# Performance work log

Measured on AMD Instinct MI355X. Metric: run time of the kernel, lower is better.

Reference implementation:

```python
import jax, jax.numpy as jnp
import numpy as np

T, H, NH, NKV, HD = 2048, 2048, 16, 4, 128
I, E, TOPK = 4096, 8, 2
EPS = 1e-5
THETA = 10000.0
NEG = -1e9


def rmsnorm(x, w):
    return x * jax.lax.rsqrt(jnp.mean(x * x, axis=-1, keepdims=True) + EPS) * w


def apply_rope(x, pos):
    # neox-style rotary: split head_dim in halves
    half = HD // 2
    inv_freq = 1.0 / (THETA ** (jnp.arange(half, dtype=jnp.float32) / half))
    f = pos.astype(jnp.float32)[:, None] * inv_freq[None, :]      # [T, half]
    cos = jnp.cos(f)[:, None, :]
    sin = jnp.sin(f)[:, None, :]
    x1, x2 = jnp.split(x, 2, axis=-1)
    return jnp.concatenate([x1 * cos - x2 * sin, x2 * cos + x1 * sin], axis=-1)


def setup_inputs() -> dict:
    key = jax.random.key(0)
    ks = jax.random.split(key, 10)
    s = 0.02
    return {
        "positions": jnp.arange(T, dtype=jnp.int32),
        "hidden_states": jax.random.normal(ks[0], (T, H), jnp.float32),
        "residual": jax.random.normal(ks[1], (T, H), jnp.float32),
        "ln1_w": jnp.ones((H,), jnp.float32),
        "ln2_w": jnp.ones((H,), jnp.float32),
        "wq": jax.random.normal(ks[2], (NH * HD, H), jnp.float32) * s,
        "wk": jax.random.normal(ks[3], (NKV * HD, H), jnp.float32) * s,
        "wv": jax.random.normal(ks[4], (NKV * HD, H), jnp.float32) * s,
        "wo": jax.random.normal(ks[5], (H, NH * HD), jnp.float32) * s,
        "gate_w": jax.random.normal(ks[6], (E, H), jnp.float32) * s,
        "w1": jax.random.normal(ks[7], (E, I, H), jnp.float32) * s,
        "w3": jax.random.normal(ks[8], (E, I, H), jnp.float32) * s,
        "w2": jax.random.normal(ks[9], (E, H, I), jnp.float32) * s,
    }


def reference(positions, hidden_states, residual, ln1_w, ln2_w,
              wq, wk, wv, wo, gate_w, w1, w3, w2):
    # fused add + input RMSNorm (vLLM RMSNorm with residual)
    x = hidden_states + residual
    residual = x
    h = rmsnorm(x, ln1_w)

    # attention: QKV proj, RoPE, GQA causal attention, o_proj
    q = (h @ wq.T).reshape(T, NH, HD)
    k = (h @ wk.T).reshape(T, NKV, HD)
    v = (h @ wv.T).reshape(T, NKV, HD)
    q = apply_rope(q, positions)
    k = apply_rope(k, positions)
    rep = NH // NKV
    k = jnp.repeat(k, rep, axis=1)  # [T, NH, HD]
    v = jnp.repeat(v, rep, axis=1)
    scores = jnp.einsum('qhd,khd->hqk', q, k) * (HD ** -0.5)
    causal = jnp.tril(jnp.ones((T, T), bool))
    scores = jnp.where(causal[None, :, :], scores, NEG)
    attn = jax.nn.softmax(scores, axis=-1)
    o = jnp.einsum('hqk,khd->qhd', attn, v).reshape(T, NH * HD)
    o = o @ wo.T

    # fused add + post-attention RMSNorm
    x = o + residual
    residual = x
    h = rmsnorm(x, ln2_w)

    # MoE: router top-k (renormalized) + SwiGLU experts
    logits = h @ gate_w.T                       # [T, E]
    probs = jax.nn.softmax(logits, axis=-1)
    top_w, top_i = jax.lax.top_k(probs, TOPK)
    top_w = top_w / jnp.sum(top_w, axis=-1, keepdims=True)
    coef = jnp.zeros((T, E), h.dtype).at[jnp.arange(T)[:, None], top_i].set(top_w)
    out = jnp.zeros_like(h)
    for e in range(E):
        g = h @ w1[e].T                          # [T, I]
        u = h @ w3[e].T
        out = out + coef[:, e:e + 1] * ((jax.nn.silu(g) * u) @ w2[e].T)
    return (out, residual)
```

## Files before the change

### kernel.cpp

```cpp
#include <hip/hip_runtime.h>
#include <hip/hip_bf16.h>
#include <math.h>


#define T_  2048
#define H_  2048
#define NH  16
#define NKV 4
#define HD  128
#define II_ 4096
#define NE  8
#define EPS 1e-5f
#define PROWS 6144

typedef __bf16 bf16x8 __attribute__((ext_vector_type(8)));
typedef float  f32x4  __attribute__((ext_vector_type(4)));
typedef unsigned short u16;

__device__ __forceinline__ u16 f2b(float f){ __bf16 b = (__bf16)f; return __builtin_bit_cast(u16, b); }
__device__ __forceinline__ float b2f(u16 u){ return (float)__builtin_bit_cast(__bf16, u); }

__device__ __forceinline__ void gll16(const void* g, void* l){
  __builtin_amdgcn_global_load_lds(
      (const __attribute__((address_space(1))) unsigned int*)g,
      (__attribute__((address_space(3))) unsigned int*)l, 16, 0, 0);
}

__global__ __launch_bounds__(256) void mx_cvt_split(const float* __restrict__ s,
                                                    u16* __restrict__ hi,
                                                    u16* __restrict__ lo, int n8)
{
  int i = blockIdx.x*256 + threadIdx.x;
  int stride = gridDim.x*256;
  for (; i < n8; i += stride){
    const f32x4* p = (const f32x4*)s + 2*(size_t)i;
    f32x4 a = p[0], b = p[1];
    uint4 uh, ul;
    u16 h0,h1,h2,h3;
    h0=f2b(a[0]); h1=f2b(a[1]); h2=f2b(a[2]); h3=f2b(a[3]);
    uh.x = (unsigned)h0 | ((unsigned)h1<<16);
    uh.y = (unsigned)h2 | ((unsigned)h3<<16);
    ul.x = (unsigned)f2b(a[0]-b2f(h0)) | ((unsigned)f2b(a[1]-b2f(h1))<<16);
    ul.y = (unsigned)f2b(a[2]-b2f(h2)) | ((unsigned)f2b(a[3]-b2f(h3))<<16);
    h0=f2b(b[0]); h1=f2b(b[1]); h2=f2b(b[2]); h3=f2b(b[3]);
    uh.z = (unsigned)h0 | ((unsigned)h1<<16);
    uh.w = (unsigned)h2 | ((unsigned)h3<<16);
    ul.z = (unsigned)f2b(b[0]-b2f(h0)) | ((unsigned)f2b(b[1]-b2f(h1))<<16);
    ul.w = (unsigned)f2b(b[2]-b2f(h2)) | ((unsigned)f2b(b[3]-b2f(h3))<<16);
    ((uint4*)hi)[i] = uh;
    ((uint4*)lo)[i] = ul;
  }
}

__global__ void mx_rope_table(const int* __restrict__ pos, float* __restrict__ cosT,
                              float* __restrict__ sinT)
{
  int i = blockIdx.x*256 + threadIdx.x;
  int t = i >> 6, d = i & 63;
  float inv = (float)exp(-((double)d/64.0) * 9.210340371976184);
  float f = (float)pos[t] * inv;
  cosT[i] = cosf(f); sinT[i] = sinf(f);
}

__global__ __launch_bounds__(256) void mx_addnorm(
    const float* __restrict__ a, const float* __restrict__ b,
    const float* __restrict__ gam, float* __restrict__ res_out,
    u16* __restrict__ hi, u16* __restrict__ lo,
    float* __restrict__ hf, u16* __restrict__ hbf, int* __restrict__ mz)
{
  int t = blockIdx.x, tid = threadIdx.x;
  if (mz && t == 0 && tid < 8) mz[tid] = 0;
  const float4* A4 = (const float4*)a + (size_t)t*512;
  const float4* B4 = (const float4*)b + (size_t)t*512;
  float4 va = A4[tid], vb = B4[tid];
  float4 x0; x0.x=va.x+vb.x; x0.y=va.y+vb.y; x0.z=va.z+vb.z; x0.w=va.w+vb.w;
  va = A4[tid+256]; vb = B4[tid+256];
  float4 x1; x1.x=va.x+vb.x; x1.y=va.y+vb.y; x1.z=va.z+vb.z; x1.w=va.w+vb.w;
  float ss = x0.x*x0.x + x0.y*x0.y + x0.z*x0.z + x0.w*x0.w
           + x1.x*x1.x + x1.y*x1.y + x1.z*x1.z + x1.w*x1.w;
  #pragma unroll
  for (int d=32; d; d>>=1) ss += __shfl_down(ss, d);
  __shared__ float red[4];
  if ((tid&63)==0) red[tid>>6] = ss;
  __syncthreads();
  ss = red[0]+red[1]+red[2]+red[3];
  float scale = rsqrtf(ss * (1.f/2048.f) + EPS);
  float4* R4 = (float4*)res_out + (size_t)t*512;
  R4[tid] = x0; R4[tid+256] = x1;
  const float4* G4p = (const float4*)gam;
  float4 g0 = G4p[tid], g1 = G4p[tid+256];
  float4 y0; y0.x=x0.x*scale*g0.x; y0.y=x0.y*scale*g0.y; y0.z=x0.z*scale*g0.z; y0.w=x0.w*scale*g0.w;
  float4 y1; y1.x=x1.x*scale*g1.x; y1.y=x1.y*scale*g1.y; y1.z=x1.z*scale*g1.z; y1.w=x1.w*scale*g1.w;
  if (hf){ float4* H4 = (float4*)hf + (size_t)t*512; H4[tid]=y0; H4[tid+256]=y1; }
  if (hi){
    ushort4 uh, ul;
    uh.x=f2b(y0.x); ul.x=f2b(y0.x-b2f(uh.x));
    uh.y=f2b(y0.y); ul.y=f2b(y0.y-b2f(uh.y));
    uh.z=f2b(y0.z); ul.z=f2b(y0.z-b2f(uh.z));
    uh.w=f2b(y0.w); ul.w=f2b(y0.w-b2f(uh.w));
    ((ushort4*)hi)[(size_t)t*512 + tid] = uh; ((ushort4*)lo)[(size_t)t*512 + tid] = ul;
    uh.x=f2b(y1.x); ul.x=f2b(y1.x-b2f(uh.x));
    uh.y=f2b(y1.y); ul.y=f2b(y1.y-b2f(uh.y));
    uh.z=f2b(y1.z); ul.z=f2b(y1.z-b2f(uh.z));
    uh.w=f2b(y1.w); ul.w=f2b(y1.w-b2f(uh.w));
    ((ushort4*)hi)[(size_t)t*512 + tid+256] = uh; ((ushort4*)lo)[(size_t)t*512 + tid+256] = ul;
  }
  if (hbf){
    ushort4 u0; u0.x=f2b(y0.x); u0.y=f2b(y0.y); u0.z=f2b(y0.z); u0.w=f2b(y0.w);
    ushort4 u1; u1.x=f2b(y1.x); u1.y=f2b(y1.y); u1.z=f2b(y1.z); u1.w=f2b(y1.w);
    ((ushort4*)hbf)[(size_t)t*512 + tid] = u0; ((ushort4*)hbf)[(size_t)t*512 + tid+256] = u1;
  }
}

template<int NX, int NY>
__global__ __launch_bounds__(256,2) void mx_gemm3g(
    const u16* __restrict__ Ah, const u16* __restrict__ Al,
    const u16* __restrict__ Bh, const u16* __restrict__ Bl,
    float* __restrict__ C, int ldc, int K)
{
  __shared__ u16 AhS[128*64], AlS[128*64], BhS[128*64], BlS[128*64];
  int bid = blockIdx.x;
  int xcd = bid & 7, j = bid >> 3;
  int x = j % NX, p = j / NX;
  int y = xcd + 8*p;
  int m0 = x*128, n0 = y*128;
  int tid = threadIdx.x;
  int w = tid>>6, lane = tid&63, wr = w>>1, wc = w&1, g = lane>>4, lr = lane&15;
  f32x4 acc[4][4];
  #pragma unroll
  for (int fm=0;fm<4;fm++)
    #pragma unroll
    for (int fn=0;fn<4;fn++) acc[fm][fn] = (f32x4){0.f,0.f,0.f,0.f};

  for (int k0 = 0; k0 < K; k0 += 64) {
    #pragma unroll
    for (int i=0;i<4;i++){
      int c = i*256 + tid, r = c>>3, ch = c&7;
      int sw = ((ch ^ (r&7))<<3);
      int db = (i*256 + w*64)<<3;
      gll16(Ah + (size_t)(m0+r)*K + k0 + sw, &AhS[db]);
      gll16(Al + (size_t)(m0+r)*K + k0 + sw, &AlS[db]);
      gll16(Bh + (size_t)(n0+r)*K + k0 + sw, &BhS[db]);
      gll16(Bl + (size_t)(n0+r)*K + k0 + sw, &BlS[db]);
    }
    __syncthreads();
    #pragma unroll
    for (int kk=0;kk<2;kk++){
      bf16x8 ah[4], al[4], bh[4], bl[4];
      #pragma unroll
      for (int fm=0;fm<4;fm++){
        int r = wr*64 + fm*16 + lr;
        int ch = ((kk<<2)+g) ^ (r&7);
        ah[fm] = *(const bf16x8*)(&AhS[(r<<6)+(ch<<3)]);
        al[fm] = *(const bf16x8*)(&AlS[(r<<6)+(ch<<3)]);
      }
      #pragma unroll
      for (int fn=0;fn<4;fn++){
        int r = wc*64 + fn*16 + lr;
        int ch = ((kk<<2)+g) ^ (r&7);
        bh[fn] = *(const bf16x8*)(&BhS[(r<<6)+(ch<<3)]);
        bl[fn] = *(const bf16x8*)(&BlS[(r<<6)+(ch<<3)]);
      }
      __builtin_amdgcn_s_setprio(1);
      #pragma unroll
      for (int fm=0;fm<4;fm++)
        #pragma unroll
        for (int fn=0;fn<4;fn++){
          acc[fm][fn] = __builtin_amdgcn_mfma_f32_16x16x32_bf16(ah[fm], bh[fn], acc[fm][fn],0,0,0);
          acc[fm][fn] = __builtin_amdgcn_mfma_f32_16x16x32_bf16(ah[fm], bl[fn], acc[fm][fn],0,0,0);
          acc[fm][fn] = __builtin_amdgcn_mfma_f32_16x16x32_bf16(al[fm], bh[fn], acc[fm][fn],0,0,0);
        }
      __builtin_amdgcn_s_setprio(0);
    }
    __syncthreads();
  }
  #pragma unroll
  for (int fm=0;fm<4;fm++)
    #pragma unroll
    for (int fn=0;fn<4;fn++)
      #pragma unroll
      for (int i=0;i<4;i++){
        size_t rg = (size_t)(m0 + wr*64 + fm*16 + g*4 + i);
        int cg = n0 + wc*64 + fn*16 + lr;
        C[rg*ldc + cg] = acc[fm][fn][i];
      }
}

template<int NY>
__global__ __launch_bounds__(256,2) void mx_moe_w13(
    const u16* __restrict__ A,
    const u16* __restrict__ B1, const u16* __restrict__ B3,
    u16* __restrict__ Y,
    const int* __restrict__ row_map, const int* __restrict__ meta)
{
  __shared__ u16 As[128*64], B1s[128*64], B3s[128*64];
  int bid = blockIdx.x;
  int xcd = bid & 7, j = bid >> 3;
  int x = j & 15, p = j >> 4;
  int panel = xcd + 8*p;
  int e = panel / NY, y = panel % NY;
  if (x >= meta[16+e]) return;
  int rowbase = meta[8+e] + (x<<7);
  const u16* B1p = B1 + ((size_t)e*II_ + y*128)*H_;
  const u16* B3p = B3 + ((size_t)e*II_ + y*128)*H_;
  int tid = threadIdx.x;
  int w = tid>>6, lane = tid&63, wr = w>>1, wc = w&1, g = lane>>4, lr = lane&15;

  f32x4 acc1[4][4], acc3[4][4];
  #pragma unroll
  for (int fm=0;fm<4;fm++)
    #pragma unroll
    for (int fn=0;fn<4;fn++){ acc1[fm][fn]=(f32x4){0,0,0,0}; acc3[fm][fn]=(f32x4){0,0,0,0}; }

  for (int k0 = 0; k0 < H_; k0 += 64) {
    #pragma unroll
    for (int i=0;i<4;i++){
      int c = i*256 + tid, r = c>>3, ch = c&7;
      int sw = (ch ^ (r&7))<<3;
      int db = (i*256 + w*64)<<3;
      int grow = row_map[rowbase + r];
      gll16(A   + (size_t)grow*H_ + k0 + sw, &As[db]);
      gll16(B1p + (size_t)r*H_    + k0 + sw, &B1s[db]);
      gll16(B3p + (size_t)r*H_    + k0 + sw, &B3s[db]);
    }
    __syncthreads();
    #pragma unroll
    for (int kk=0;kk<2;kk++){
      bf16x8 af[4], b1f[4], b3f[4];
      #pragma unroll
      for (int fm=0;fm<4;fm++){
        int r = wr*64 + fm*16 + lr;
        int ch = ((kk<<2)+g) ^ (r&7);
        af[fm] = *(const bf16x8*)(&As[(r<<6)+(ch<<3)]);
      }
      #pragma unroll
      for (int fn=0;fn<4;fn++){
        int r = wc*64 + fn*16 + lr;
        int ch = ((kk<<2)+g) ^ (r&7);
        b1f[fn] = *(const bf16x8*)(&B1s[(r<<6)+(ch<<3)]);
        b3f[fn] = *(const bf16x8*)(&B3s[(r<<6)+(ch<<3)]);
      }
      __builtin_amdgcn_s_setprio(1);
      #pragma unroll
      for (int fm=0;fm<4;fm++)
        #pragma unroll
        for (int fn=0;fn<4;fn++){
          acc1[fm][fn] = __builtin_amdgcn_mfma_f32_16x16x32_bf16(af[fm], b1f[fn], acc1[fm][fn],0,0,0);
          acc3[fm][fn] = __builtin_amdgcn_mfma_f32_16x16x32_bf16(af[fm], b3f[fn], acc3[fm][fn],0,0,0);
        }
      __builtin_amdgcn_s_setprio(0);
    }
    __syncthreads();
  }
  int n0 = y*128 + wc*64;
  #pragma unroll
  for (int fm=0;fm<4;fm++)
    #pragma unroll
    for (int fn=0;fn<4;fn++)
      #pragma unroll
      for (int i=0;i<4;i++){
        size_t rg = (size_t)(rowbase + wr*64 + fm*16 + g*4 + i);
        int cg = n0 + fn*16 + lr;
        float gg = acc1[fm][fn][i], uu = acc3[fm][fn][i];
        float sg = gg / (1.f + __expf(-gg));
        Y[rg*II_ + cg] = f2b(sg * uu);
      }
}

template<int NY>
__global__ __launch_bounds__(256,2) void mx_moe_w2k(
    const u16* __restrict__ A,
    const u16* __restrict__ B,
    u16* __restrict__ C,
    const int* __restrict__ meta)
{
  __shared__ u16 As[128*64], Bs[128*64];
  int bid = blockIdx.x;
  int xcd = bid & 7, j = bid >> 3;
  int x = j & 15, p = j >> 4;
  int panel = xcd + 8*p;
  int e = panel / NY, y = panel % NY;
  if (x >= meta[16+e]) return;
  int rowbase = meta[8+e] + (x<<7);
  const u16* Bp = B + ((size_t)e*H_ + y*128)*II_;
  int tid = threadIdx.x;
  int w = tid>>6, lane = tid&63, wr = w>>1, wc = w&1, g = lane>>4, lr = lane&15;

  f32x4 acc[4][4];
  #pragma unroll
  for (int fm=0;fm<4;fm++)
    #pragma unroll
    for (int fn=0;fn<4;fn++) acc[fm][fn] = (f32x4){0,0,0,0};

  for (int k0 = 0; k0 < II_; k0 += 64) {
    #pragma unroll
    for (int i=0;i<4;i++){
      int c = i*256 + tid, r = c>>3, ch = c&7;
      int sw = (ch ^ (r&7))<<3;
      int db = (i*256 + w*64)<<3;
      gll16(A  + (size_t)(rowbase + r)*II_ + k0 + sw, &As[db]);
      gll16(Bp + (size_t)r*II_             + k0 + sw, &Bs[db]);
    }
    __syncthreads();
    #pragma unroll
    for (int kk=0;kk<2;kk++){
      bf16x8 af[4], bf[4];
      #pragma unroll
      for (int fm=0;fm<4;fm++){
        int r = wr*64 + fm*16 + lr;
        int ch = ((kk<<2)+g) ^ (r&7);
        af[fm] = *(const bf16x8*)(&As[(r<<6)+(ch<<3)]);
      }
      #pragma unroll
      for (int fn=0;fn<4;fn++){
        int r = wc*64 + fn*16 + lr;
        int ch = ((kk<<2)+g) ^ (r&7);
        bf[fn] = *(const bf16x8*)(&Bs[(r<<6)+(ch<<3)]);
      }
      __builtin_amdgcn_s_setprio(1);
      #pragma unroll
      for (int fm=0;fm<4;fm++)
        #pragma unroll
        for (int fn=0;fn<4;fn++)
          acc[fm][fn] = __builtin_amdgcn_mfma_f32_16x16x32_bf16(af[fm], bf[fn], acc[fm][fn],0,0,0);
      __builtin_amdgcn_s_setprio(0);
    }
    __syncthreads();
  }
  int n0 = y*128 + wc*64;
  #pragma unroll
  for (int fm=0;fm<4;fm++)
    #pragma unroll
    for (int fn=0;fn<4;fn++)
      #pragma unroll
      for (int i=0;i<4;i++){
        size_t rg = (size_t)(rowbase + wr*64 + fm*16 + g*4 + i);
        int cg = n0 + fn*16 + lr;
        C[rg*H_ + cg] = f2b(acc[fm][fn][i]);
      }
}

__global__ __launch_bounds__(256) void mx_rope_apply(const float* __restrict__ qkv,
    const float* __restrict__ cosT, const float* __restrict__ sinT,
    u16* __restrict__ qh, u16* __restrict__ ql, u16* __restrict__ kh, u16* __restrict__ kl)
{
  int t = blockIdx.x*4 + (threadIdx.x>>6);
  int hh = blockIdx.y, d = threadIdx.x & 63;
  const float* row = qkv + (size_t)t*3072;
  float c = cosT[t*64+d], s = sinT[t*64+d];
  float x1, x2; size_t base; u16 *oh, *ol;
  if (hh < NH){ x1 = row[hh*HD+d]; x2 = row[hh*HD+d+64];
     base = ((size_t)hh*T_ + t)*HD; oh = qh; ol = ql; }
  else { int kvh = hh-NH; x1 = row[2048 + kvh*HD + d]; x2 = row[2048 + kvh*HD + d + 64];
     base = ((size_t)kvh*T_ + t)*HD; oh = kh; ol = kl; }
  float o1 = x1*c - x2*s, o2 = x2*c + x1*s;
  u16 a = f2b(o1); oh[base+d]    = a; ol[base+d]    = f2b(o1 - b2f(a));
  u16 b = f2b(o2); oh[base+d+64] = b; ol[base+d+64] = f2b(o2 - b2f(b));
}

__global__ void mx_transpose_v(const float* __restrict__ qkv,
                               u16* __restrict__ vh, u16* __restrict__ vl)
{
  __shared__ float tile[64][132];
  int kv = blockIdx.x, t0 = blockIdx.y*64, tid = threadIdx.x;
  #pragma unroll
  for (int it=0; it<32; ++it){
    int idx = it*256 + tid; int r = idx>>7, d = idx&127;
    tile[r][d] = qkv[(size_t)(t0+r)*3072 + 2560 + kv*HD + d];
  }
  __syncthreads();
  #pragma unroll
  for (int it=0; it<32; ++it){
    int idx = it*256 + tid; int d = idx>>6, j = idx&63;
    float x = tile[j][d];
    u16 a = f2b(x);
    size_t o = ((size_t)kv*HD + d)*T_ + t0 + j;
    vh[o] = a; vl[o] = f2b(x - b2f(a));
  }
}

__global__ __launch_bounds__(512) void mx_attn(
  const u16* __restrict__ qh_, const u16* __restrict__ ql_,
  const u16* __restrict__ kh_, const u16* __restrict__ kl_,
  const u16* __restrict__ vh_, const u16* __restrict__ vl_,
  u16* __restrict__ oh_, u16* __restrict__ ol_,
  const float* __restrict__ w1f, const float* __restrict__ w3f,
  const float* __restrict__ w2f,
  u16* __restrict__ w1b, u16* __restrict__ w3b, u16* __restrict__ w2b)
{
  if (blockIdx.y >= 8){
    const int n8 = NE*II_*H_/8;
    int hb = (blockIdx.y - 8)*gridDim.x + blockIdx.x;
    int i  = hb*512 + threadIdx.x;
    const int stride = 3840*512;
    for (; i < 3*n8; i += stride){
      const float* s; u16* d; int j;
      if (i < n8)        { s = w1f; d = w1b; j = i; }
      else if (i < 2*n8) { s = w3f; d = w3b; j = i - n8; }
      else               { s = w2f; d = w2b; j = i - 2*n8; }
      const f32x4* p = (const f32x4*)s + 2*(size_t)j;
      f32x4 a = p[0], b = p[1];
      uint4 u;
      u.x = (unsigned)f2b(a[0]) | ((unsigned)f2b(a[1])<<16);
      u.y = (unsigned)f2b(a[2]) | ((unsigned)f2b(a[3])<<16);
      u.z = (unsigned)f2b(b[0]) | ((unsigned)f2b(b[1])<<16);
      u.w = (unsigned)f2b(b[2]) | ((unsigned)f2b(b[3])<<16);
      ((uint4*)d)[j] = u;
    }
    return;
  }

  int pair = blockIdx.y;
  int kvh = pair >> 1;
  int qt = (pair & 4) ? (31 - (int)blockIdx.x) : (int)blockIdx.x;
  int tid = threadIdx.x, w = tid>>6, lane = tid&63, g = lane>>4, lr = lane&15;
  int head = pair*2 + (w>>2);
  int q0 = qt*64 + (w&3)*16;
  __shared__ u16 KV[2][4][8192];
  __shared__ u16 Ph[8][1024], Pl[8][1024];

  bf16x8 qfh[4], qfl[4];
  const u16* qrh = qh_ + ((size_t)head*T_ + q0 + lr)*HD;
  const u16* qrl = ql_ + ((size_t)head*T_ + q0 + lr)*HD;
  #pragma unroll
  for (int kk=0;kk<4;kk++){
    qfh[kk] = *(const bf16x8*)(qrh + kk*32 + g*8);
    qfl[kk] = *(const bf16x8*)(qrl + kk*32 + g*8);
  }
  f32x4 o[8];
  #pragma unroll
  for (int nf=0;nf<8;nf++) o[nf] = (f32x4){0.f,0.f,0.f,0.f};
  float mreg[4] = {-3e38f,-3e38f,-3e38f,-3e38f}, lsum[4] = {0.f,0.f,0.f,0.f};

  const u16* kbase = kh_ + (size_t)kvh*T_*HD;
  const u16* lbase = kl_ + (size_t)kvh*T_*HD;
  const u16* vbase = vh_ + (size_t)kvh*HD*T_;
  const u16* wbase = vl_ + (size_t)kvh*HD*T_;

  auto stage = [&](int buf, int kvb){
    #pragma unroll
    for (int i=0;i<2;i++){
      int cb = i*512 + w*64;
      int c  = cb + lane;
      int kr = c>>4, kc = ((c&15) ^ (kr&7))<<3;
      gll16(kbase + (size_t)(kvb+kr)*HD + kc, &KV[buf][0][cb*8]);
      gll16(lbase + (size_t)(kvb+kr)*HD + kc, &KV[buf][1][cb*8]);
      int vr = c>>3, vc = ((c&7) ^ (vr&7))<<3;
      gll16(vbase + (size_t)vr*T_ + kvb + vc, &KV[buf][2][cb*8]);
      gll16(wbase + (size_t)vr*T_ + kvb + vc, &KV[buf][3][cb*8]);
    }
  };

  stage(0, 0);

  for (int kt = 0; kt <= qt; ++kt) {
    int cur = kt & 1;
    int kvb = kt*64;
    if (kt < qt) {
      stage(cur^1, kvb+64);
      asm volatile("s_waitcnt vmcnt(8)" ::: "memory");
    } else {
      asm volatile("s_waitcnt vmcnt(0)" ::: "memory");
    }
    __builtin_amdgcn_s_barrier();

    f32x4 s[4];
    #pragma unroll
    for (int nf=0;nf<4;nf++) s[nf] = (f32x4){0.f,0.f,0.f,0.f};
    __builtin_amdgcn_s_setprio(1);
    #pragma unroll
    for (int nf=0; nf<4; nf++){
      int row = nf*16 + lr;
      #pragma unroll
      for (int kk=0;kk<4;kk++){
        int off = row*128 + ((((kk<<2)+g) ^ (lr&7))<<3);
        bf16x8 kf = *(const bf16x8*)(&KV[cur][0][off]);
        bf16x8 kg = *(const bf16x8*)(&KV[cur][1][off]);
        s[nf] = __builtin_amdgcn_mfma_f32_16x16x32_bf16(qfh[kk], kf, s[nf],0,0,0);
        s[nf] = __builtin_amdgcn_mfma_f32_16x16x32_bf16(qfh[kk], kg, s[nf],0,0,0);
        s[nf] = __builtin_amdgcn_mfma_f32_16x16x32_bf16(qfl[kk], kf, s[nf],0,0,0);
      }
    }
    __builtin_amdgcn_s_setprio(0);

    float sv[4][4], pm[4];
    #pragma unroll
    for (int i=0;i<4;i++) pm[i] = -3e38f;
    bool diag = (kt == qt);
    #pragma unroll
    for (int nf=0;nf<4;nf++)
      #pragma unroll
      for (int i=0;i<4;i++){
        float v = s[nf][i] * 0.08838834764831845f;
        if (diag && (kvb + nf*16 + lr > q0 + g*4 + i)) v = -1e30f;
        sv[nf][i] = v;
        pm[i] = fmaxf(pm[i], v);
      }
    #pragma unroll
    for (int i=0;i<4;i++)
      #pragma unroll
      for (int d=1; d<16; d<<=1) pm[i] = fmaxf(pm[i], __shfl_xor(pm[i], d));
    float sf[4], psum[4];
    #pragma unroll
    for (int i=0;i<4;i++){
      float nm = fmaxf(mreg[i], pm[i]);
      sf[i] = __expf(mreg[i] - nm);
      mreg[i] = nm; psum[i] = 0.f;
    }
    #pragma unroll
    for (int nf=0;nf<4;nf++)
      #pragma unroll
      for (int i=0;i<4;i++){
        float e = __expf(sv[nf][i] - mreg[i]);
        sv[nf][i] = e; psum[i] += e;
      }
    #pragma unroll
    for (int i=0;i<4;i++){
      #pragma unroll
      for (int d=1; d<16; d<<=1) psum[i] += __shfl_xor(psum[i], d);
      lsum[i] = lsum[i]*sf[i] + psum[i];
    }
    #pragma unroll
    for (int nf=0;nf<8;nf++)
      #pragma unroll
      for (int i=0;i<4;i++) o[nf][i] *= sf[i];

    #pragma unroll
    for (int nf=0;nf<4;nf++)
      #pragma unroll
      for (int i=0;i<4;i++){
        int qi = g*4 + i, kv = nf*16 + lr;
        int idx = qi*64 + (kv ^ ((qi&7)<<3));
        u16 hb = f2b(sv[nf][i]);
        Ph[w][idx] = hb;
        Pl[w][idx] = f2b(sv[nf][i] - b2f(hb));
      }

    #pragma unroll
    for (int kk2=0; kk2<2; kk2++){
      int pidx = lr*64 + ((kk2*32 + g*8) ^ ((lr&7)<<3));
      bf16x8 ph = *(const bf16x8*)(&Ph[w][pidx]);
      bf16x8 pl = *(const bf16x8*)(&Pl[w][pidx]);
      __builtin_amdgcn_s_setprio(1);
      #pragma unroll
      for (int nf=0; nf<8; nf++){
        int row = nf*16 + lr;
        int off = row*64 + ((((kk2<<2)+g) ^ (lr&7))<<3);
        bf16x8 vf = *(const bf16x8*)(&KV[cur][2][off]);
        bf16x8 vg = *(const bf16x8*)(&KV[cur][3][off]);
        o[nf] = __builtin_amdgcn_mfma_f32_16x16x32_bf16(ph, vf, o[nf],0,0,0);
        o[nf] = __builtin_amdgcn_mfma_f32_16x16x32_bf16(ph, vg, o[nf],0,0,0);
        o[nf] = __builtin_amdgcn_mfma_f32_16x16x32_bf16(pl, vf, o[nf],0,0,0);
      }
      __builtin_amdgcn_s_setprio(0);
    }
    __builtin_amdgcn_s_barrier();
  }

  float inv[4];
  #pragma unroll
  for (int i=0;i<4;i++) inv[i] = 1.0f / lsum[i];
  #pragma unroll
  for (int nf=0;nf<8;nf++)
    #pragma unroll
    for (int i=0;i<4;i++){
      float v = o[nf][i] * inv[i];
      size_t oidx = (size_t)(q0 + g*4 + i)*2048 + head*HD + nf*16 + lr;
      u16 hb = f2b(v);
      oh_[oidx] = hb; ol_[oidx] = f2b(v - b2f(hb));
    }
}

__global__ __launch_bounds__(256) void mx_router(
    const float* __restrict__ h2, const float* __restrict__ gw,
    int* __restrict__ meta, int* __restrict__ tki, float* __restrict__ tkw)
{
  int t = blockIdx.x, tid = threadIdx.x;
  float p[8] = {0,0,0,0,0,0,0,0};
  const float* row = h2 + (size_t)t*H_;
  for (int i = tid; i < H_; i += 256) {
    float x = row[i];
    #pragma unroll
    for (int e=0;e<8;e++) p[e] += x * gw[e*H_ + i];
  }
  #pragma unroll
  for (int e=0;e<8;e++)
    #pragma unroll
    for (int d=32; d; d>>=1) p[e] += __shfl_down(p[e], d);
  __shared__ float red[4][8];
  int w = tid>>6;
  if ((tid&63)==0){
    #pragma unroll
    for (int e=0;e<8;e++) red[w][e] = p[e];
  }
  __syncthreads();
  if (tid==0){
    float lg[8];
    #pragma unroll
    for (int e=0;e<8;e++) lg[e] = red[0][e]+red[1][e]+red[2][e]+red[3][e];
    int e0 = 0;
    for (int e=1;e<8;e++) if (lg[e] > lg[e0]) e0 = e;
    int e1 = (e0==0)?1:0;
    for (int e=0;e<8;e++) if (e!=e0 && lg[e] > lg[e1]) e1 = e;
    float w0 = 1.f/(1.f + __expf(lg[e1]-lg[e0]));
    tki[t*2]=e0; tki[t*2+1]=e1; tkw[t*2]=w0; tkw[t*2+1]=1.f-w0;
    atomicAdd(&meta[e0],1); atomicAdd(&meta[e1],1);
  }
}

__global__ void mx_scan(int* __restrict__ meta, int* __restrict__ perm, int gsh)
{
  if (threadIdx.x == 0){
    int run = 0;
    for (int e=0;e<8;e++){
      meta[8+e] = run;
      int pt = (meta[e] + (1<<gsh) - 1) >> gsh;
      meta[16+e] = pt;
      run += pt << gsh;
      meta[24+e] = 0;
    }
  }
  for (int i = threadIdx.x; i < PROWS; i += 256) perm[i] = 0;
}

__global__ void mx_scatter(const int* __restrict__ tki, int* __restrict__ meta,
                           int* __restrict__ perm, int* __restrict__ slot)
{
  int t = blockIdx.x*256 + threadIdx.x;
  if (t >= T_) return;
  #pragma unroll
  for (int j=0;j<2;j++){
    int e = tki[t*2+j];
    int s = atomicAdd(&meta[24+e], 1);
    int pos = meta[8+e] + s;
    perm[pos] = t;
    slot[t*2+j] = pos;
  }
}

__global__ void mx_combine(const u16* __restrict__ Y2, const int* __restrict__ slot,
                           const float* __restrict__ tkw, float* __restrict__ out)
{
  int t = blockIdx.x, tid = threadIdx.x;
  int s0 = slot[t*2], s1 = slot[t*2+1];
  float w0 = tkw[t*2], w1 = tkw[t*2+1];
  const uint4* r0 = (const uint4*)(Y2 + (size_t)s0*H_);
  const uint4* r1 = (const uint4*)(Y2 + (size_t)s1*H_);
  float4* o4 = (float4*)(out + (size_t)t*H_);
  for (int i = tid; i < 256; i += 256){
    uint4 a = r0[i], b = r1[i];
    const u16* ap = (const u16*)&a;
    const u16* bp = (const u16*)&b;
    float4 c0, c1;
    c0.x = w0*b2f(ap[0]) + w1*b2f(bp[0]);
    c0.y = w0*b2f(ap[1]) + w1*b2f(bp[1]);
    c0.z = w0*b2f(ap[2]) + w1*b2f(bp[2]);
    c0.w = w0*b2f(ap[3]) + w1*b2f(bp[3]);
    c1.x = w0*b2f(ap[4]) + w1*b2f(bp[4]);
    c1.y = w0*b2f(ap[5]) + w1*b2f(bp[5]);
    c1.z = w0*b2f(ap[6]) + w1*b2f(bp[6]);
    c1.w = w0*b2f(ap[7]) + w1*b2f(bp[7]);
    o4[i*2]   = c0;
    o4[i*2+1] = c1;
  }
}

extern "C" void kernel_launch(void* const* d_in, const int* in_sizes, int n_in,
                              void* d_out, int out_size, void* d_ws, size_t ws_size,
                              hipStream_t stream)
{
  (void)in_sizes; (void)n_in; (void)out_size;
  const int*   positions = (const int*)  d_in[0];
  const float* hidden    = (const float*)d_in[1];
  const float* residual  = (const float*)d_in[2];
  const float* ln1       = (const float*)d_in[3];
  const float* ln2       = (const float*)d_in[4];
  const float* wq        = (const float*)d_in[5];
  const float* wk        = (const float*)d_in[6];
  const float* wv        = (const float*)d_in[7];
  const float* wo        = (const float*)d_in[8];
  const float* gatew     = (const float*)d_in[9];
  const float* w1        = (const float*)d_in[10];
  const float* w3        = (const float*)d_in[11];
  const float* w2        = (const float*)d_in[12];
  float* outp = (float*)d_out;
  char* ws = (char*)d_ws;

  size_t off = 0;
  auto alloc = [&](size_t n){ size_t o = off; off += (n + 255) & ~(size_t)255; return o; };
  float* cosT = (float*)(ws + alloc((size_t)T_*64*4));
  float* sinT = (float*)(ws + alloc((size_t)T_*64*4));
  size_t res1_off = alloc((size_t)T_*H_*4);
  float* res1 = (float*)(ws + res1_off);
  u16*   h1h  = (u16*)  (ws + alloc((size_t)T_*H_*2));
  u16*   h1l  = (u16*)  (ws + alloc((size_t)T_*H_*2));
  float* qkvF = (float*)(ws + alloc((size_t)T_*3072*4));
  size_t qh_off = alloc((size_t)NH*T_*HD*2);
  u16*   qh   = (u16*)  (ws + qh_off);
  u16*   ql   = (u16*)  (ws + alloc((size_t)NH*T_*HD*2));
  u16*   kh   = (u16*)  (ws + alloc((size_t)NKV*T_*HD*2));
  u16*   kl   = (u16*)  (ws + alloc((size_t)NKV*T_*HD*2));
  u16*   vh   = (u16*)  (ws + alloc((size_t)NKV*T_*HD*2));
  u16*   vl   = (u16*)  (ws + alloc((size_t)NKV*T_*HD*2));
  u16*   aoh  = (u16*)  (ws + alloc((size_t)T_*2048*2));
  u16*   aol  = (u16*)  (ws + alloc((size_t)T_*2048*2));
  float* oF   = (float*)(ws + alloc((size_t)T_*H_*4));
  float* h2f  = (float*)(ws + alloc((size_t)T_*H_*4));
  u16*   h2b  = (u16*)  (ws + alloc((size_t)T_*H_*2));
  int*   meta = (int*)  (ws + alloc(32*4));
  int*   tki  = (int*)  (ws + alloc((size_t)T_*2*4));
  float* tkw  = (float*)(ws + alloc((size_t)T_*2*4));
  int*   slot = (int*)  (ws + alloc((size_t)T_*2*4));
  int*   perm = (int*)  (ws + alloc((size_t)PROWS*4));
  u16*   Y1   = (u16*)  (ws + alloc((size_t)PROWS*II_*2));
  u16*   Y2   = (u16*)(ws + qh_off);
  u16* w1b = (u16*)(ws + alloc((size_t)NE*II_*H_*2));
  u16* w3b = (u16*)(ws + alloc((size_t)NE*II_*H_*2));
  u16* w2b = (u16*)(ws + alloc((size_t)NE*H_*II_*2));
  u16* qwh = (u16*)(ws + alloc((size_t)3072*H_*2));
  u16* qwl = (u16*)(ws + alloc((size_t)3072*H_*2));
  u16* woh = (u16*)(ws + alloc((size_t)H_*H_*2));
  u16* wol = (u16*)(ws + alloc((size_t)H_*H_*2));

  mx_cvt_split<<<512, 256, 0, stream>>>(wq, qwh,             qwl,             2048*2048/8);
  mx_cvt_split<<<512, 256, 0, stream>>>(wk, qwh + 2048*2048, qwl + 2048*2048, 512*2048/8);
  mx_cvt_split<<<512, 256, 0, stream>>>(wv, qwh + 2560*2048, qwl + 2560*2048, 512*2048/8);
  mx_cvt_split<<<512, 256, 0, stream>>>(wo, woh,             wol,             2048*2048/8);
  mx_rope_table<<<512, 256, 0, stream>>>(positions, cosT, sinT);
  mx_addnorm<<<T_, 256, 0, stream>>>(hidden, residual, ln1, res1, h1h, h1l,
                                     nullptr, nullptr, nullptr);
  mx_gemm3g<16,24><<<384, 256, 0, stream>>>(h1h, h1l, qwh, qwl, qkvF, 3072, H_);
  mx_rope_apply<<<dim3(T_/4, NH+NKV), 256, 0, stream>>>(qkvF, cosT, sinT, qh, ql, kh, kl);
  mx_transpose_v<<<dim3(NKV, T_/64), 256, 0, stream>>>(qkvF, vh, vl);
  mx_attn<<<dim3(T_/64, 128), 512, 0, stream>>>(qh, ql, kh, kl, vh, vl, aoh, aol,
                                                w1, w3, w2, w1b, w3b, w2b);
  mx_gemm3g<16,16><<<256, 256, 0, stream>>>(aoh, aol, woh, wol, oF, 2048, 2048);
  mx_addnorm<<<T_, 256, 0, stream>>>(oF, res1, ln2, outp + (size_t)T_*H_,
                                     nullptr, nullptr, h2f, h2b, meta);
  mx_router<<<T_, 256, 0, stream>>>(h2f, gatew, meta, tki, tkw);
  mx_scan<<<1, 256, 0, stream>>>(meta, perm, 7);
  mx_scatter<<<T_/256, 256, 0, stream>>>(tki, meta, perm, slot);
  mx_moe_w13<32><<<4096, 256, 0, stream>>>(h2b, w1b, w3b, Y1, perm, meta);
  mx_moe_w2k<16><<<2048, 256, 0, stream>>>(Y1, w2b, Y2, meta);
  mx_combine<<<T_, 256, 0, stream>>>(Y2, slot, tkw, outp);
  (void)ws_size;
}
```

Measured before the change: 1.004 ms.

## Fuse small kernels: weight conversion, rope+V transpose, addnorm+router

Merges the four weight split-conversion launches into one kernel, fuses RoPE application with the V transpose into a single launch, and folds the MoE router logits and top-2 selection into the second add+RMSNorm kernel. The router now reads the normalized activations from registers instead of a float32 buffer, so that buffer's write and read disappear. Expert-count zeroing moves to the first addnorm. The goal is fewer launches and less global memory traffic, at the cost of more branching and idle blocks in the rope/transpose grid.

```diff
diff --git a/kernel.cpp b/kernel.cpp
--- a/kernel.cpp
+++ b/kernel.cpp
@@ -26,14 +26,23 @@
       (__attribute__((address_space(3))) unsigned int*)l, 16, 0, 0);
 }
 
-__global__ __launch_bounds__(256) void mx_cvt_split(const float* __restrict__ s,
-                                                    u16* __restrict__ hi,
-                                                    u16* __restrict__ lo, int n8)
-{
+__global__ __launch_bounds__(256) void mx_cvt_split4(
+    const float* __restrict__ wq, const float* __restrict__ wk,
+    const float* __restrict__ wv, const float* __restrict__ wo,
+    u16* __restrict__ qwh, u16* __restrict__ qwl,
+    u16* __restrict__ woh, u16* __restrict__ wol)
+{
+  const int nq = 2048*2048/8, nk = 512*2048/8;
+  const int total = nq + nk + nk + nq;
   int i = blockIdx.x*256 + threadIdx.x;
   int stride = gridDim.x*256;
-  for (; i < n8; i += stride){
-    const f32x4* p = (const f32x4*)s + 2*(size_t)i;
+  for (; i < total; i += stride){
+    const float* s; u16 *hi, *lo; int j;
+    if (i < nq)            { s = wq; hi = qwh;             lo = qwl;             j = i; }
+    else if (i < nq+nk)    { s = wk; hi = qwh + 2048*2048; lo = qwl + 2048*2048; j = i - nq; }
+    else if (i < nq+2*nk)  { s = wv; hi = qwh + 2560*2048; lo = qwl + 2560*2048; j = i - nq - nk; }
+    else                   { s = wo; hi = woh;             lo = wol;             j = i - nq - 2*nk; }
+    const f32x4* p = (const f32x4*)s + 2*(size_t)j;
     f32x4 a = p[0], b = p[1];
     uint4 uh, ul;
     u16 h0,h1,h2,h3;
@@ -47,8 +56,8 @@
     uh.w = (unsigned)h2 | ((unsigned)h3<<16);
     ul.z = (unsigned)f2b(b[0]-b2f(h0)) | ((unsigned)f2b(b[1]-b2f(h1))<<16);
     ul.w = (unsigned)f2b(b[2]-b2f(h2)) | ((unsigned)f2b(b[3]-b2f(h3))<<16);
-    ((uint4*)hi)[i] = uh;
-    ((uint4*)lo)[i] = ul;
+    ((uint4*)hi)[j] = uh;
+    ((uint4*)lo)[j] = ul;
   }
 }
 
@@ -65,8 +74,7 @@
 __global__ __launch_bounds__(256) void mx_addnorm(
     const float* __restrict__ a, const float* __restrict__ b,
     const float* __restrict__ gam, float* __restrict__ res_out,
-    u16* __restrict__ hi, u16* __restrict__ lo,
-    float* __restrict__ hf, u16* __restrict__ hbf, int* __restrict__ mz)
+    u16* __restrict__ hi, u16* __restrict__ lo, int* __restrict__ mz)
 {
   int t = blockIdx.x, tid = threadIdx.x;
   if (mz && t == 0 && tid < 8) mz[tid] = 0;
@@ -91,24 +99,83 @@
   float4 g0 = G4p[tid], g1 = G4p[tid+256];
   float4 y0; y0.x=x0.x*scale*g0.x; y0.y=x0.y*scale*g0.y; y0.z=x0.z*scale*g0.z; y0.w=x0.w*scale*g0.w;
   float4 y1; y1.x=x1.x*scale*g1.x; y1.y=x1.y*scale*g1.y; y1.z=x1.z*scale*g1.z; y1.w=x1.w*scale*g1.w;
-  if (hf){ float4* H4 = (float4*)hf + (size_t)t*512; H4[tid]=y0; H4[tid+256]=y1; }
-  if (hi){
-    ushort4 uh, ul;
-    uh.x=f2b(y0.x); ul.x=f2b(y0.x-b2f(uh.x));
-    uh.y=f2b(y0.y); ul.y=f2b(y0.y-b2f(uh.y));
-    uh.z=f2b(y0.z); ul.z=f2b(y0.z-b2f(uh.z));
-    uh.w=f2b(y0.w); ul.w=f2b(y0.w-b2f(uh.w));
-    ((ushort4*)hi)[(size_t)t*512 + tid] = uh; ((ushort4*)lo)[(size_t)t*512 + tid] = ul;
-    uh.x=f2b(y1.x); ul.x=f2b(y1.x-b2f(uh.x));
-    uh.y=f2b(y1.y); ul.y=f2b(y1.y-b2f(uh.y));
-    uh.z=f2b(y1.z); ul.z=f2b(y1.z-b2f(uh.z));
-    uh.w=f2b(y1.w); ul.w=f2b(y1.w-b2f(uh.w));
-    ((ushort4*)hi)[(size_t)t*512 + tid+256] = uh; ((ushort4*)lo)[(size_t)t*512 + tid+256] = ul;
-  }
-  if (hbf){
-    ushort4 u0; u0.x=f2b(y0.x); u0.y=f2b(y0.y); u0.z=f2b(y0.z); u0.w=f2b(y0.w);
-    ushort4 u1; u1.x=f2b(y1.x); u1.y=f2b(y1.y); u1.z=f2b(y1.z); u1.w=f2b(y1.w);
-    ((ushort4*)hbf)[(size_t)t*512 + tid] = u0; ((ushort4*)hbf)[(size_t)t*512 + tid+256] = u1;
+  ushort4 uh, ul;
+  uh.x=f2b(y0.x); ul.x=f2b(y0.x-b2f(uh.x));
+  uh.y=f2b(y0.y); ul.y=f2b(y0.y-b2f(uh.y));
+  uh.z=f2b(y0.z); ul.z=f2b(y0.z-b2f(uh.z));
+  uh.w=f2b(y0.w); ul.w=f2b(y0.w-b2f(uh.w));
+  ((ushort4*)hi)[(size_t)t*512 + tid] = uh; ((ushort4*)lo)[(size_t)t*512 + tid] = ul;
+  uh.x=f2b(y1.x); ul.x=f2b(y1.x-b2f(uh.x));
+  uh.y=f2b(y1.y); ul.y=f2b(y1.y-b2f(uh.y));
+  uh.z=f2b(y1.z); ul.z=f2b(y1.z-b2f(uh.z));
+  uh.w=f2b(y1.w); ul.w=f2b(y1.w-b2f(uh.w));
+  ((ushort4*)hi)[(size_t)t*512 + tid+256] = uh; ((ushort4*)lo)[(size_t)t*512 + tid+256] = ul;
+}
+
+__global__ __launch_bounds__(256) void mx_addnorm_router(
+    const float* __restrict__ a, const float* __restrict__ b,
+    const float* __restrict__ gam, float* __restrict__ res_out,
+    u16* __restrict__ hbf,
+    const float* __restrict__ gw, int* __restrict__ meta,
+    int* __restrict__ tki, float* __restrict__ tkw)
+{
+  int t = blockIdx.x, tid = threadIdx.x;
+  const float4* A4 = (const float4*)a + (size_t)t*512;
+  const float4* B4 = (const float4*)b + (size_t)t*512;
+  float4 va = A4[tid], vb = B4[tid];
+  float4 x0; x0.x=va.x+vb.x; x0.y=va.y+vb.y; x0.z=va.z+vb.z; x0.w=va.w+vb.w;
+  va = A4[tid+256]; vb = B4[tid+256];
+  float4 x1; x1.x=va.x+vb.x; x1.y=va.y+vb.y; x1.z=va.z+vb.z; x1.w=va.w+vb.w;
+  float ss = x0.x*x0.x + x0.y*x0.y + x0.z*x0.z + x0.w*x0.w
+           + x1.x*x1.x + x1.y*x1.y + x1.z*x1.z + x1.w*x1.w;
+  #pragma unroll
+  for (int d=32; d; d>>=1) ss += __shfl_down(ss, d);
+  __shared__ float red[4];
+  __shared__ float redr[4][8];
+  if ((tid&63)==0) red[tid>>6] = ss;
+  __syncthreads();
+  ss = red[0]+red[1]+red[2]+red[3];
+  float scale = rsqrtf(ss * (1.f/2048.f) + EPS);
+  float4* R4 = (float4*)res_out + (size_t)t*512;
+  R4[tid] = x0; R4[tid+256] = x1;
+  const float4* G4p = (const float4*)gam;
+  float4 g0 = G4p[tid], g1 = G4p[tid+256];
+  float4 y0; y0.x=x0.x*scale*g0.x; y0.y=x0.y*scale*g0.y; y0.z=x0.z*scale*g0.z; y0.w=x0.w*scale*g0.w;
+  float4 y1; y1.x=x1.x*scale*g1.x; y1.y=x1.y*scale*g1.y; y1.z=x1.z*scale*g1.z; y1.w=x1.w*scale*g1.w;
+  ushort4 u0; u0.x=f2b(y0.x); u0.y=f2b(y0.y); u0.z=f2b(y0.z); u0.w=f2b(y0.w);
+  ushort4 u1; u1.x=f2b(y1.x); u1.y=f2b(y1.y); u1.z=f2b(y1.z); u1.w=f2b(y1.w);
+  ((ushort4*)hbf)[(size_t)t*512 + tid] = u0; ((ushort4*)hbf)[(size_t)t*512 + tid+256] = u1;
+
+  const float4* GW = (const float4*)gw;
+  float p[8];
+  #pragma unroll
+  for (int e=0;e<8;e++){
+    float4 ga = GW[e*512 + tid];
+    float4 gb = GW[e*512 + 256 + tid];
+    p[e] = y0.x*ga.x + y0.y*ga.y + y0.z*ga.z + y0.w*ga.w
+         + y1.x*gb.x + y1.y*gb.y + y1.z*gb.z + y1.w*gb.w;
+  }
+  #pragma unroll
+  for (int e=0;e<8;e++)
+    #pragma unroll
+    for (int d=32; d; d>>=1) p[e] += __shfl_down(p[e], d);
+  int w = tid>>6;
+  if ((tid&63)==0){
+    #pragma unroll
+    for (int e=0;e<8;e++) redr[w][e] = p[e];
+  }
+  __syncthreads();
+  if (tid==0){
+    float lg[8];
+    #pragma unroll
+    for (int e=0;e<8;e++) lg[e] = redr[0][e]+redr[1][e]+redr[2][e]+redr[3][e];
+    int e0 = 0;
+    for (int e=1;e<8;e++) if (lg[e] > lg[e0]) e0 = e;
+    int e1 = (e0==0)?1:0;
+    for (int e=0;e<8;e++) if (e!=e0 && lg[e] > lg[e1]) e1 = e;
+    float w0 = 1.f/(1.f + __expf(lg[e1]-lg[e0]));
+    tki[t*2]=e0; tki[t*2+1]=e1; tkw[t*2]=w0; tkw[t*2+1]=1.f-w0;
+    atomicAdd(&meta[e0],1); atomicAdd(&meta[e1],1);
   }
 }
 
@@ -340,29 +407,30 @@
       }
 }
 
-__global__ __launch_bounds__(256) void mx_rope_apply(const float* __restrict__ qkv,
+__global__ __launch_bounds__(256) void mx_rope_trans(const float* __restrict__ qkv,
     const float* __restrict__ cosT, const float* __restrict__ sinT,
-    u16* __restrict__ qh, u16* __restrict__ ql, u16* __restrict__ kh, u16* __restrict__ kl)
-{
-  int t = blockIdx.x*4 + (threadIdx.x>>6);
-  int hh = blockIdx.y, d = threadIdx.x & 63;
-  const float* row = qkv + (size_t)t*3072;
-  float c = cosT[t*64+d], s = sinT[t*64+d];
-  float x1, x2; size_t base; u16 *oh, *ol;
-  if (hh < NH){ x1 = row[hh*HD+d]; x2 = row[hh*HD+d+64];
-     base = ((size_t)hh*T_ + t)*HD; oh = qh; ol = ql; }
-  else { int kvh = hh-NH; x1 = row[2048 + kvh*HD + d]; x2 = row[2048 + kvh*HD + d + 64];
-     base = ((size_t)kvh*T_ + t)*HD; oh = kh; ol = kl; }
-  float o1 = x1*c - x2*s, o2 = x2*c + x1*s;
-  u16 a = f2b(o1); oh[base+d]    = a; ol[base+d]    = f2b(o1 - b2f(a));
-  u16 b = f2b(o2); oh[base+d+64] = b; ol[base+d+64] = f2b(o2 - b2f(b));
-}
-
-__global__ void mx_transpose_v(const float* __restrict__ qkv,
-                               u16* __restrict__ vh, u16* __restrict__ vl)
+    u16* __restrict__ qh, u16* __restrict__ ql, u16* __restrict__ kh, u16* __restrict__ kl,
+    u16* __restrict__ vh, u16* __restrict__ vl)
 {
   __shared__ float tile[64][132];
-  int kv = blockIdx.x, t0 = blockIdx.y*64, tid = threadIdx.x;
+  int yb = blockIdx.y;
+  if (yb < NH+NKV){
+    int t = blockIdx.x*4 + (threadIdx.x>>6);
+    int hh = yb, d = threadIdx.x & 63;
+    const float* row = qkv + (size_t)t*3072;
+    float c = cosT[t*64+d], s = sinT[t*64+d];
+    float x1, x2; size_t base; u16 *oh, *ol;
+    if (hh < NH){ x1 = row[hh*HD+d]; x2 = row[hh*HD+d+64];
+       base = ((size_t)hh*T_ + t)*HD; oh = qh; ol = ql; }
+    else { int kvh = hh-NH; x1 = row[2048 + kvh*HD + d]; x2 = row[2048 + kvh*HD + d + 64];
+       base = ((size_t)kvh*T_ + t)*HD; oh = kh; ol = kl; }
+    float o1 = x1*c - x2*s, o2 = x2*c + x1*s;
+    u16 a = f2b(o1); oh[base+d]    = a; ol[base+d]    = f2b(o1 - b2f(a));
+    u16 b = f2b(o2); oh[base+d+64] = b; ol[base+d+64] = f2b(o2 - b2f(b));
+    return;
+  }
+  if ((int)blockIdx.x >= T_/64) return;
+  int kv = yb - (NH+NKV), t0 = blockIdx.x*64, tid = threadIdx.x;
   #pragma unroll
   for (int it=0; it<32; ++it){
     int idx = it*256 + tid; int r = idx>>7, d = idx&127;
@@ -571,43 +639,6 @@
     }
 }
 
-__global__ __launch_bounds__(256) void mx_router(
-    const float* __restrict__ h2, const float* __restrict__ gw,
-    int* __restrict__ meta, int* __restrict__ tki, float* __restrict__ tkw)
-{
-  int t = blockIdx.x, tid = threadIdx.x;
-  float p[8] = {0,0,0,0,0,0,0,0};
-  const float* row = h2 + (size_t)t*H_;
-  for (int i = tid; i < H_; i += 256) {
-    float x = row[i];
-    #pragma unroll
-    for (int e=0;e<8;e++) p[e] += x * gw[e*H_ + i];
-  }
-  #pragma unroll
-  for (int e=0;e<8;e++)
-    #pragma unroll
-    for (int d=32; d; d>>=1) p[e] += __shfl_down(p[e], d);
-  __shared__ float red[4][8];
-  int w = tid>>6;
-  if ((tid&63)==0){
-    #pragma unroll
-    for (int e=0;e<8;e++) red[w][e] = p[e];
-  }
-  __syncthreads();
-  if (tid==0){
-    float lg[8];
-    #pragma unroll
-    for (int e=0;e<8;e++) lg[e] = red[0][e]+red[1][e]+red[2][e]+red[3][e];
-    int e0 = 0;
-    for (int e=1;e<8;e++) if (lg[e] > lg[e0]) e0 = e;
-    int e1 = (e0==0)?1:0;
-    for (int e=0;e<8;e++) if (e!=e0 && lg[e] > lg[e1]) e1 = e;
-    float w0 = 1.f/(1.f + __expf(lg[e1]-lg[e0]));
-    tki[t*2]=e0; tki[t*2+1]=e1; tkw[t*2]=w0; tkw[t*2+1]=1.f-w0;
-    atomicAdd(&meta[e0],1); atomicAdd(&meta[e1],1);
-  }
-}
-
 __global__ void mx_scan(int* __restrict__ meta, int* __restrict__ perm, int gsh)
 {
   if (threadIdx.x == 0){
@@ -647,7 +678,8 @@
   const uint4* r0 = (const uint4*)(Y2 + (size_t)s0*H_);
   const uint4* r1 = (const uint4*)(Y2 + (size_t)s1*H_);
   float4* o4 = (float4*)(out + (size_t)t*H_);
-  for (int i = tid; i < 256; i += 256){
+  {
+    int i = tid;
     uint4 a = r0[i], b = r1[i];
     const u16* ap = (const u16*)&a;
     const u16* bp = (const u16*)&b;
@@ -705,7 +737,6 @@
   u16*   aoh  = (u16*)  (ws + alloc((size_t)T_*2048*2));
   u16*   aol  = (u16*)  (ws + alloc((size_t)T_*2048*2));
   float* oF   = (float*)(ws + alloc((size_t)T_*H_*4));
-  float* h2f  = (float*)(ws + alloc((size_t)T_*H_*4));
   u16*   h2b  = (u16*)  (ws + alloc((size_t)T_*H_*2));
   int*   meta = (int*)  (ws + alloc(32*4));
   int*   tki  = (int*)  (ws + alloc((size_t)T_*2*4));
@@ -722,22 +753,17 @@
   u16* woh = (u16*)(ws + alloc((size_t)H_*H_*2));
   u16* wol = (u16*)(ws + alloc((size_t)H_*H_*2));
 
-  mx_cvt_split<<<512, 256, 0, stream>>>(wq, qwh,             qwl,             2048*2048/8);
-  mx_cvt_split<<<512, 256, 0, stream>>>(wk, qwh + 2048*2048, qwl + 2048*2048, 512*2048/8);
-  mx_cvt_split<<<512, 256, 0, stream>>>(wv, qwh + 2560*2048, qwl + 2560*2048, 512*2048/8);
-  mx_cvt_split<<<512, 256, 0, stream>>>(wo, woh,             wol,             2048*2048/8);
+  mx_cvt_split4<<<1024, 256, 0, stream>>>(wq, wk, wv, wo, qwh, qwl, woh, wol);
   mx_rope_table<<<512, 256, 0, stream>>>(positions, cosT, sinT);
-  mx_addnorm<<<T_, 256, 0, stream>>>(hidden, residual, ln1, res1, h1h, h1l,
-                                     nullptr, nullptr, nullptr);
+  mx_addnorm<<<T_, 256, 0, stream>>>(hidden, residual, ln1, res1, h1h, h1l, meta);
   mx_gemm3g<16,24><<<384, 256, 0, stream>>>(h1h, h1l, qwh, qwl, qkvF, 3072, H_);
-  mx_rope_apply<<<dim3(T_/4, NH+NKV), 256, 0, stream>>>(qkvF, cosT, sinT, qh, ql, kh, kl);
-  mx_transpose_v<<<dim3(NKV, T_/64), 256, 0, stream>>>(qkvF, vh, vl);
+  mx_rope_trans<<<dim3(T_/4, NH+NKV+NKV), 256, 0, stream>>>(qkvF, cosT, sinT,
+                                                            qh, ql, kh, kl, vh, vl);
   mx_attn<<<dim3(T_/64, 128), 512, 0, stream>>>(qh, ql, kh, kl, vh, vl, aoh, aol,
                                                 w1, w3, w2, w1b, w3b, w2b);
   mx_gemm3g<16,16><<<256, 256, 0, stream>>>(aoh, aol, woh, wol, oF, 2048, 2048);
-  mx_addnorm<<<T_, 256, 0, stream>>>(oF, res1, ln2, outp + (size_t)T_*H_,
-                                     nullptr, nullptr, h2f, h2b, meta);
-  mx_router<<<T_, 256, 0, stream>>>(h2f, gatew, meta, tki, tkw);
+  mx_addnorm_router<<<T_, 256, 0, stream>>>(oF, res1, ln2, outp + (size_t)T_*H_,
+                                            h2b, gatew, meta, tki, tkw);
   mx_scan<<<1, 256, 0, stream>>>(meta, perm, 7);
   mx_scatter<<<T_/256, 256, 0, stream>>>(tki, meta, perm, slot);
   mx_moe_w13<32><<<4096, 256, 0, stream>>>(h2b, w1b, w3b, Y1, perm, meta);
```

New measurement: 976.8 us. 2.7% less time.
